# Optimization experiments

Measured on AMD Instinct MI355X. Metric: run time of the kernel, lower is better.

The kernel has to match this reference:

```python
import jax, jax.numpy as jnp
import numpy as np

ENCODER_DIM, DECODER_DIM, ATTENTION_DIM = 2048, 512, 512
B, L = 128, 196


def setup_inputs() -> dict:
    key = jax.random.key(0)
    ks = jax.random.split(key, 8)
    s_u = 1.0 / np.sqrt(ENCODER_DIM)
    s_w = 1.0 / np.sqrt(DECODER_DIM)
    s_a = 1.0 / np.sqrt(ATTENTION_DIM)
    return {
        "features": jax.random.normal(ks[0], (B, L, ENCODER_DIM), jnp.float32),
        "hidden_state": jax.random.normal(ks[1], (B, DECODER_DIM), jnp.float32),
        "U_w": jax.random.uniform(ks[2], (ENCODER_DIM, ATTENTION_DIM), jnp.float32, -s_u, s_u),
        "U_b": jax.random.uniform(ks[3], (ATTENTION_DIM,), jnp.float32, -s_u, s_u),
        "W_w": jax.random.uniform(ks[4], (DECODER_DIM, ATTENTION_DIM), jnp.float32, -s_w, s_w),
        "W_b": jax.random.uniform(ks[5], (ATTENTION_DIM,), jnp.float32, -s_w, s_w),
        "A_w": jax.random.uniform(ks[6], (ATTENTION_DIM,), jnp.float32, -s_a, s_a),
        "A_b": jax.random.uniform(ks[7], (1,), jnp.float32, -s_a, s_a),
    }


def reference(features, hidden_state, U_w, U_b, W_w, W_b, A_w, A_b):
    # u_hs: [B, L, A], w_ah: [B, A]
    u_hs = jnp.einsum('ble,ea->bla', features, U_w) + U_b
    w_ah = hidden_state @ W_w + W_b
    combined = jnp.tanh(u_hs + w_ah[:, None, :])          # [B, L, A]
    scores = jnp.einsum('bla,a->bl', combined, A_w) + A_b[0]  # [B, L]
    alpha = jax.nn.softmax(scores, axis=1)                 # [B, L]
    context = jnp.einsum('bl,ble->be', alpha, features)    # [B, E]
    return alpha, context
```

## Files before the change

kernel.cpp:

```cpp
#include <hip/hip_runtime.h>
#include <hip/hip_bf16.h>

#define ENC 2048
#define ADIM 512
#define DEC 512
#define NBATCH 128
#define NL 196
#define MTOT (NBATCH * NL)
#define NKT 32
#define NPART 32

typedef __attribute__((ext_vector_type(8))) short short8;
typedef __attribute__((ext_vector_type(4))) float f32x4;
typedef __attribute__((ext_vector_type(4))) unsigned int u32x4;

__device__ __forceinline__ unsigned short f2bf(float f) {
    __hip_bfloat16 h = __float2bfloat16(f);
    union { __hip_bfloat16 h; unsigned short u; } cv; cv.h = h; return cv.u;
}
__device__ __forceinline__ unsigned int f2bf2(float lo, float hi) {
    __hip_bfloat162 h = __float22bfloat162_rn(float2{lo, hi});
    union { __hip_bfloat162 h; unsigned int u; } cv; cv.h = h; return cv.u;
}

__device__ __forceinline__ void load_lds16(const void* g, void* l) {
    __builtin_amdgcn_global_load_lds(
        (const __attribute__((address_space(1))) unsigned int*)g,
        (__attribute__((address_space(3))) unsigned int*)l, 16, 0, 0);
}

__global__ void wah_kernel(const float* __restrict__ hidden, const float* __restrict__ Ww,
                           const float* __restrict__ Wb, float* __restrict__ wah) {
    __shared__ __align__(16) float hs[DEC];
    const int b = blockIdx.x, a = threadIdx.x;
    hs[a] = hidden[b * DEC + a];
    __syncthreads();
    float acc = Wb[a];
    #pragma unroll 4
    for (int d = 0; d < DEC; d += 4) {
        f32x4 h = *(const f32x4*)&hs[d];
        acc += h.x * Ww[(d    ) * ADIM + a];
        acc += h.y * Ww[(d + 1) * ADIM + a];
        acc += h.z * Ww[(d + 2) * ADIM + a];
        acc += h.w * Ww[(d + 3) * ADIM + a];
    }
    wah[b * ADIM + a] = acc;
}

__global__ void transpose_uw(const float* __restrict__ Uw, unsigned short* __restrict__ uwT) {
    __shared__ float t[32][33];
    const int k0 = blockIdx.x * 32, n0 = blockIdx.y * 32;
    const int tx = threadIdx.x, ty = threadIdx.y;
    #pragma unroll
    for (int i = 0; i < 4; ++i)
        t[ty + 8 * i][tx] = Uw[(size_t)(k0 + ty + 8 * i) * ADIM + n0 + tx];
    __syncthreads();
    #pragma unroll
    for (int i = 0; i < 4; ++i)
        uwT[(size_t)(n0 + ty + 8 * i) * ENC + k0 + tx] = f2bf(t[tx][ty + 8 * i]);
}

__global__ __launch_bounds__(256, 4) void gemm_score_kernel(
    const float* __restrict__ feat, const unsigned short* __restrict__ uwT,
    const float* __restrict__ Ub, const float* __restrict__ wahb,
    const float* __restrict__ Aw, float* __restrict__ part)
{
    __shared__ __align__(16) unsigned char As[8192];
    __shared__ __align__(16) unsigned char Bs[16384];

    const int tid  = threadIdx.x;
    const int lane = tid & 63;
    const int w    = tid >> 6;
    const int l15  = lane & 15, ldr = lane >> 4;

    const int bid  = blockIdx.x;
    const int work = (bid & 7) * 196 + (bid >> 3);
    const int mb   = work >> 2;
    const int nbk  = work & 3;

    const int r_ = tid >> 2, kq = tid & 3;
    const float* aSrc = feat + (size_t)(mb * 64 + r_) * ENC + kq * 16;
    const int wA0 = r_ * 128 + (((kq * 2    ) ^ (r_ & 7)) << 4);
    const int wA1 = r_ * 128 + (((kq * 2 + 1) ^ (r_ & 7)) << 4);

    const unsigned short* bSrc = uwT
        + (size_t)(nbk * 128 + w * 32 + (lane >> 3)) * ENC
        + (((lane & 7) ^ ((lane >> 3) & 7)) << 3);

    int abyte[4][2], bbyte[2][2];
    #pragma unroll
    for (int ks = 0; ks < 2; ++ks) {
        const int sl = ((ks * 4 + ldr) ^ (l15 & 7)) << 4;
        #pragma unroll
        for (int f = 0; f < 4; ++f)
            abyte[f][ks] = (f * 16 + l15) * 128 + sl;
        #pragma unroll
        for (int g = 0; g < 2; ++g)
            bbyte[g][ks] = (w * 32 + g * 16 + l15) * 128 + sl;
    }

    f32x4 acc[4][2];
    #pragma unroll
    for (int i = 0; i < 4; ++i)
        #pragma unroll
        for (int j = 0; j < 2; ++j)
            acc[i][j] = (f32x4){0.f, 0.f, 0.f, 0.f};

    #pragma unroll 1
    for (int kt = 0; kt < NKT; ++kt) {
        const f32x4* p = (const f32x4*)(aSrc + (size_t)kt * 64);
        f32x4 a0 = p[0], a1 = p[1], a2 = p[2], a3 = p[3];
        #pragma unroll
        for (int c = 0; c < 4; ++c)
            load_lds16(bSrc + (size_t)kt * 64 + c * 8 * ENC, Bs + w * 4096 + c * 1024);
        u32x4 w0, w1;
        w0.x = f2bf2(a0.x, a0.y); w0.y = f2bf2(a0.z, a0.w);
        w0.z = f2bf2(a1.x, a1.y); w0.w = f2bf2(a1.z, a1.w);
        w1.x = f2bf2(a2.x, a2.y); w1.y = f2bf2(a2.z, a2.w);
        w1.z = f2bf2(a3.x, a3.y); w1.w = f2bf2(a3.z, a3.w);
        *(u32x4*)(As + wA0) = w0;
        *(u32x4*)(As + wA1) = w1;
        __syncthreads();

        #pragma unroll
        for (int ks = 0; ks < 2; ++ks) {
            short8 af[4], bf[2];
            #pragma unroll
            for (int f = 0; f < 4; ++f) af[f] = *(const short8*)(As + abyte[f][ks]);
            #pragma unroll
            for (int g = 0; g < 2; ++g) bf[g] = *(const short8*)(Bs + bbyte[g][ks]);
            #pragma unroll
            for (int fm = 0; fm < 4; ++fm)
                #pragma unroll
                for (int g = 0; g < 2; ++g)
                    acc[fm][g] = __builtin_amdgcn_mfma_f32_16x16x32_bf16(
                        af[fm], bf[g], acc[fm][g], 0, 0, 0);
        }
        __syncthreads();
    }

    float ub2[2], aw2[2]; int cidx[2];
    #pragma unroll
    for (int g = 0; g < 2; ++g) {
        const int c = nbk * 128 + w * 32 + g * 16 + l15;
        cidx[g] = c; ub2[g] = Ub[c]; aw2[g] = Aw[c];
    }
    #pragma unroll
    for (int fm = 0; fm < 4; ++fm) {
        #pragma unroll
        for (int r = 0; r < 4; ++r) {
            const int m = mb * 64 + fm * 16 + ldr * 4 + r;
            const int b = m / NL;
            const float* wrow = wahb + b * ADIM;
            #pragma unroll
            for (int g = 0; g < 2; ++g) {
                float s = aw2[g] * tanhf(acc[fm][g][r] + ub2[g] + wrow[cidx[g]]);
                s += __shfl_xor(s, 1);
                s += __shfl_xor(s, 2);
                s += __shfl_xor(s, 4);
                s += __shfl_xor(s, 8);
                if (l15 == 0) part[(nbk * 8 + w * 2 + g) * MTOT + m] = s;
            }
        }
    }
}

__global__ void softmax_kernel(const float* __restrict__ part, const float* __restrict__ Ab,
                               float* __restrict__ alpha) {
    const int b = blockIdx.x, t = threadIdx.x;
    float sv = 0.f;
    if (t < NL) {
        sv = Ab[0];
        #pragma unroll 8
        for (int p = 0; p < NPART; ++p) sv += part[p * MTOT + b * NL + t];
    }
    float v = (t < NL) ? sv : -3.4e38f;
    #pragma unroll
    for (int o = 32; o >= 1; o >>= 1) v = fmaxf(v, __shfl_xor(v, o));
    __shared__ float rm[4], rs[4];
    if ((t & 63) == 0) rm[t >> 6] = v;
    __syncthreads();
    const float bm = fmaxf(fmaxf(rm[0], rm[1]), fmaxf(rm[2], rm[3]));
    const float e = (t < NL) ? expf(sv - bm) : 0.f;
    float s = e;
    #pragma unroll
    for (int o = 32; o >= 1; o >>= 1) s += __shfl_xor(s, o);
    if ((t & 63) == 0) rs[t >> 6] = s;
    __syncthreads();
    const float bs = rs[0] + rs[1] + rs[2] + rs[3];
    if (t < NL) alpha[b * NL + t] = e / bs;
}

__global__ void context_kernel(const float* __restrict__ feat, const float* __restrict__ alpha,
                               float* __restrict__ ctx) {
    __shared__ float al[NL];
    const int b = blockIdx.x, chunk = blockIdx.y, t = threadIdx.x;
    for (int i = t; i < NL; i += 128) al[i] = alpha[b * NL + i];
    __syncthreads();
    const int e0 = chunk * 512 + t * 4;
    const float* fp = feat + (size_t)b * NL * ENC + e0;
    f32x4 acc0 = (f32x4){0.f, 0.f, 0.f, 0.f};
    f32x4 acc1 = (f32x4){0.f, 0.f, 0.f, 0.f};
    #pragma unroll 2
    for (int l = 0; l < NL; l += 2) {
        f32x4 f0 = *(const f32x4*)(fp + (size_t)l * ENC);
        f32x4 f1 = *(const f32x4*)(fp + (size_t)(l + 1) * ENC);
        acc0 += al[l] * f0;
        acc1 += al[l + 1] * f1;
    }
    f32x4 rsum = acc0 + acc1;
    *(f32x4*)(ctx + (size_t)b * ENC + e0) = rsum;
}

extern "C" void kernel_launch(void* const* d_in, const int* in_sizes, int n_in,
                              void* d_out, int out_size, void* d_ws, size_t ws_size,
                              hipStream_t stream) {
    const float* feat   = (const float*)d_in[0];
    const float* hidden = (const float*)d_in[1];
    const float* Uw     = (const float*)d_in[2];
    const float* Ub     = (const float*)d_in[3];
    const float* Ww     = (const float*)d_in[4];
    const float* Wb     = (const float*)d_in[5];
    const float* Aw     = (const float*)d_in[6];
    const float* Ab     = (const float*)d_in[7];

    float* out   = (float*)d_out;
    float* alpha = out;
    float* ctx   = out + MTOT;

    char* ws = (char*)d_ws;
    float*          wahb = (float*)ws;
    unsigned short* uwT  = (unsigned short*)(ws + 262144);
    float*          partb= (float*)(ws + 262144 + 2097152);

    wah_kernel<<<dim3(128), dim3(512), 0, stream>>>(hidden, Ww, Wb, wahb);
    transpose_uw<<<dim3(64, 16), dim3(32, 8), 0, stream>>>(Uw, uwT);
    gemm_score_kernel<<<dim3(1568), dim3(256), 0, stream>>>(feat, uwT, Ub, wahb, Aw, partb);
    softmax_kernel<<<dim3(128), dim3(256), 0, stream>>>(partb, Ab, alpha);
    context_kernel<<<dim3(128, 4), dim3(128), 0, stream>>>(feat, alpha, ctx);
}
```

Before: 169.8 us.

## Pre-convert features to bf16 and use larger 128x128 bf16 MFMA GEMM tile

Adds a pass that converts the fp32 features to a bf16 copy in the workspace. The score GEMM then streams bf16 A tiles straight into LDS with global_load_lds, using 128x128 tiles per block instead of 64-row tiles. Each block covers more columns, so the number of partial score slices falls from 32 to 8. The cost is an extra full read of the 205 MB fp32 features and a write of a 103 MB bf16 copy. This path runs only when the workspace is large enough, otherwise the old fp32 kernel is used.

```diff
diff --git a/kernel.cpp b/kernel.cpp
--- a/kernel.cpp
+++ b/kernel.cpp
@@ -8,7 +8,6 @@
 #define NL 196
 #define MTOT (NBATCH * NL)
 #define NKT 32
-#define NPART 32
 
 typedef __attribute__((ext_vector_type(8))) short short8;
 typedef __attribute__((ext_vector_type(4))) float f32x4;
@@ -27,6 +26,20 @@
     __builtin_amdgcn_global_load_lds(
         (const __attribute__((address_space(1))) unsigned int*)g,
         (__attribute__((address_space(3))) unsigned int*)l, 16, 0, 0);
+}
+
+__global__ void cvt_feat_kernel(const float* __restrict__ feat, unsigned short* __restrict__ featb) {
+    const size_t total  = (size_t)MTOT * ENC;
+    const size_t stride = (size_t)gridDim.x * blockDim.x * 8;
+    size_t i = ((size_t)blockIdx.x * blockDim.x + threadIdx.x) * 8;
+    for (; i < total; i += stride) {
+        f32x4 lo = *(const f32x4*)(feat + i);
+        f32x4 hi = *(const f32x4*)(feat + i + 4);
+        u32x4 v;
+        v.x = f2bf2(lo.x, lo.y); v.y = f2bf2(lo.z, lo.w);
+        v.z = f2bf2(hi.x, hi.y); v.w = f2bf2(hi.z, hi.w);
+        *(u32x4*)(featb + i) = v;
+    }
 }
 
 __global__ void wah_kernel(const float* __restrict__ hidden, const float* __restrict__ Ww,
@@ -60,7 +73,103 @@
         uwT[(size_t)(n0 + ty + 8 * i) * ENC + k0 + tx] = f2bf(t[tx][ty + 8 * i]);
 }
 
-__global__ __launch_bounds__(256, 4) void gemm_score_kernel(
+__global__ __launch_bounds__(256, 3) void gemm_score_bf16(
+    const unsigned short* __restrict__ featb, const unsigned short* __restrict__ uwT,
+    const float* __restrict__ Ub, const float* __restrict__ wahb,
+    const float* __restrict__ Aw, float* __restrict__ part)
+{
+    __shared__ __align__(16) unsigned char As[16384];
+    __shared__ __align__(16) unsigned char Bs[16384];
+
+    const int tid  = threadIdx.x;
+    const int lane = tid & 63;
+    const int w    = tid >> 6;
+    const int wr   = w >> 1, wc = w & 1;
+    const int l15  = lane & 15, ldr = lane >> 4;
+
+    const int bid  = blockIdx.x;
+    const int work = (bid & 7) * 98 + (bid >> 3);
+    const int mb   = work >> 2;
+    const int nbk  = work & 3;
+
+    const int swz = ((lane & 7) ^ ((lane >> 3) & 7)) << 3;
+    const unsigned short* aS = featb + (size_t)(mb  * 128 + w * 32 + (lane >> 3)) * ENC + swz;
+    const unsigned short* bS = uwT   + (size_t)(nbk * 128 + w * 32 + (lane >> 3)) * ENC + swz;
+
+    int abyte[4][2], bbyte[4][2];
+    #pragma unroll
+    for (int f = 0; f < 4; ++f) {
+        const int ra = wr * 64 + f * 16 + l15;
+        const int rb = wc * 64 + f * 16 + l15;
+        #pragma unroll
+        for (int ks = 0; ks < 2; ++ks) {
+            abyte[f][ks] = ra * 128 + (((ks * 4 + ldr) ^ (ra & 7)) << 4);
+            bbyte[f][ks] = rb * 128 + (((ks * 4 + ldr) ^ (rb & 7)) << 4);
+        }
+    }
+
+    f32x4 acc[4][4];
+    #pragma unroll
+    for (int i = 0; i < 4; ++i)
+        #pragma unroll
+        for (int j = 0; j < 4; ++j)
+            acc[i][j] = (f32x4){0.f, 0.f, 0.f, 0.f};
+
+    #pragma unroll 1
+    for (int kt = 0; kt < NKT; ++kt) {
+        #pragma unroll
+        for (int c = 0; c < 4; ++c)
+            load_lds16(aS + (size_t)kt * 64 + c * 8 * ENC, As + w * 4096 + c * 1024);
+        #pragma unroll
+        for (int c = 0; c < 4; ++c)
+            load_lds16(bS + (size_t)kt * 64 + c * 8 * ENC, Bs + w * 4096 + c * 1024);
+        __syncthreads();
+
+        #pragma unroll
+        for (int ks = 0; ks < 2; ++ks) {
+            short8 af[4], bf[4];
+            #pragma unroll
+            for (int f = 0; f < 4; ++f) {
+                af[f] = *(const short8*)(As + abyte[f][ks]);
+                bf[f] = *(const short8*)(Bs + bbyte[f][ks]);
+            }
+            #pragma unroll
+            for (int fm = 0; fm < 4; ++fm)
+                #pragma unroll
+                for (int fn = 0; fn < 4; ++fn)
+                    acc[fm][fn] = __builtin_amdgcn_mfma_f32_16x16x32_bf16(
+                        af[fm], bf[fn], acc[fm][fn], 0, 0, 0);
+        }
+        __syncthreads();
+    }
+
+    float ub4[4], aw4[4]; int cidx[4];
+    #pragma unroll
+    for (int f = 0; f < 4; ++f) {
+        const int c = nbk * 128 + wc * 64 + f * 16 + l15;
+        cidx[f] = c; ub4[f] = Ub[c]; aw4[f] = Aw[c];
+    }
+    #pragma unroll
+    for (int fm = 0; fm < 4; ++fm) {
+        #pragma unroll
+        for (int r = 0; r < 4; ++r) {
+            const int m = mb * 128 + wr * 64 + fm * 16 + ldr * 4 + r;
+            const int b = m / NL;
+            const float* wrow = wahb + b * ADIM;
+            float s = 0.f;
+            #pragma unroll
+            for (int f = 0; f < 4; ++f)
+                s += aw4[f] * tanhf(acc[fm][f][r] + ub4[f] + wrow[cidx[f]]);
+            s += __shfl_xor(s, 1);
+            s += __shfl_xor(s, 2);
+            s += __shfl_xor(s, 4);
+            s += __shfl_xor(s, 8);
+            if (l15 == 0) part[(nbk * 2 + wc) * MTOT + m] = s;
+        }
+    }
+}
+
+__global__ __launch_bounds__(256, 4) void gemm_score_fp32(
     const float* __restrict__ feat, const unsigned short* __restrict__ uwT,
     const float* __restrict__ Ub, const float* __restrict__ wahb,
     const float* __restrict__ Aw, float* __restrict__ part)
@@ -166,13 +275,12 @@
 }
 
 __global__ void softmax_kernel(const float* __restrict__ part, const float* __restrict__ Ab,
-                               float* __restrict__ alpha) {
+                               float* __restrict__ alpha, int npart) {
     const int b = blockIdx.x, t = threadIdx.x;
     float sv = 0.f;
     if (t < NL) {
         sv = Ab[0];
-        #pragma unroll 8
-        for (int p = 0; p < NPART; ++p) sv += part[p * MTOT + b * NL + t];
+        for (int p = 0; p < npart; ++p) sv += part[p * MTOT + b * NL + t];
     }
     float v = (t < NL) ? sv : -3.4e38f;
     #pragma unroll
@@ -228,14 +336,34 @@
     float* alpha = out;
     float* ctx   = out + MTOT;
 
+    const size_t FEATB_BYTES = (size_t)MTOT * ENC * 2;
+    const size_t SMALL_NEED  = 262144 + 2097152 + (size_t)32 * MTOT * 4;
+    const size_t BIG_NEED    = FEATB_BYTES + 262144 + 2097152 + (size_t)8 * MTOT * 4;
+
     char* ws = (char*)d_ws;
-    float*          wahb = (float*)ws;
-    unsigned short* uwT  = (unsigned short*)(ws + 262144);
-    float*          partb= (float*)(ws + 262144 + 2097152);
-
-    wah_kernel<<<dim3(128), dim3(512), 0, stream>>>(hidden, Ww, Wb, wahb);
-    transpose_uw<<<dim3(64, 16), dim3(32, 8), 0, stream>>>(Uw, uwT);
-    gemm_score_kernel<<<dim3(1568), dim3(256), 0, stream>>>(feat, uwT, Ub, wahb, Aw, partb);
-    softmax_kernel<<<dim3(128), dim3(256), 0, stream>>>(partb, Ab, alpha);
-    context_kernel<<<dim3(128, 4), dim3(128), 0, stream>>>(feat, alpha, ctx);
-}
+
+    if (ws_size >= BIG_NEED) {
+        unsigned short* featb = (unsigned short*)ws;
+        float*          wahb  = (float*)(ws + FEATB_BYTES);
+        unsigned short* uwT   = (unsigned short*)(ws + FEATB_BYTES + 262144);
+        float*          partb = (float*)(ws + FEATB_BYTES + 262144 + 2097152);
+
+        cvt_feat_kernel<<<dim3(2048), dim3(256), 0, stream>>>(feat, featb);
+        wah_kernel<<<dim3(128), dim3(512), 0, stream>>>(hidden, Ww, Wb, wahb);
+        transpose_uw<<<dim3(64, 16), dim3(32, 8), 0, stream>>>(Uw, uwT);
+        gemm_score_bf16<<<dim3(784), dim3(256), 0, stream>>>(featb, uwT, Ub, wahb, Aw, partb);
+        softmax_kernel<<<dim3(128), dim3(256), 0, stream>>>(partb, Ab, alpha, 8);
+        context_kernel<<<dim3(128, 4), dim3(128), 0, stream>>>(feat, alpha, ctx);
+    } else {
+        float*          wahb  = (float*)ws;
+        unsigned short* uwT   = (unsigned short*)(ws + 262144);
+        float*          partb = (float*)(ws + 262144 + 2097152);
+        (void)SMALL_NEED;
+
+        wah_kernel<<<dim3(128), dim3(512), 0, stream>>>(hidden, Ww, Wb, wahb);
+        transpose_uw<<<dim3(64, 16), dim3(32, 8), 0, stream>>>(Uw, uwT);
+        gemm_score_fp32<<<dim3(1568), dim3(256), 0, stream>>>(feat, uwT, Ub, wahb, Aw, partb);
+        softmax_kernel<<<dim3(128), dim3(256), 0, stream>>>(partb, Ab, alpha, 32);
+        context_kernel<<<dim3(128, 4), dim3(128), 0, stream>>>(feat, alpha, ctx);
+    }
+}
```

New measurement: 196.8 us. +15.9%, slower.
